# Kernel tuning notes

Measured on AMD Instinct MI355X. Metric: run time of the kernel, lower is better.

The kernel has to match this reference:

```python
import jax, jax.numpy as jnp
import numpy as np

B, H, W = 1, 180, 360
NB, BS = 8, 96
EMBED = NB * BS            # 768
LATENT = 4 * EMBED         # 3072 (mlp_ratio=4)
MODD = 64
LAM = 0.01                 # sparsity_threshold (softshrink)

def _ln(x, w, b):
    m = x.mean(-1, keepdims=True)
    v = x.var(-1, keepdims=True)
    return (x - m) * jax.lax.rsqrt(v + 1e-5) * w + b

def _gelu(x):
    return jax.nn.gelu(x, approximate=False)  # torch nn.GELU default (erf)

def _scale_shift(e, w0, b0, w1, b1):
    o = _gelu(e @ w0 + b0) @ w1 + b1
    s, t = jnp.split(o, 2, axis=1)
    return 1.0 + s, t

def _softshrink(x):
    return jnp.where(x > LAM, x - LAM, jnp.where(x < -LAM, x + LAM, 0.0))

def _bd(x, w):  # block-diagonal contraction on spectral features
    return jnp.einsum('nyxbi,bio->nyxbo', x, w)

def _filter(x, e, w1, b1, w2, b2, fs_w0, fs_b0, fs_w1, fs_b1):
    bias = x
    b, h, w, c = x.shape
    xf = jnp.fft.rfft2(x, axes=(1, 2), norm='ortho')
    wf = w // 2 + 1
    xr = xf.real.reshape(b, h, wf, NB, BS)
    xi = xf.imag.reshape(b, h, wf, NB, BS)
    tm = min(h, w) // 2 + 1
    km = tm  # hard_thresholding_fraction = 1.0
    lo, hi = tm - km, min(tm + km, h)
    xrk, xik = xr[:, lo:hi, :km], xi[:, lo:hi, :km]
    o1r = _bd(xrk, w1[0]) - _bd(xik, w1[1]) + b1[0]
    o1i = _bd(xik, w1[0]) + _bd(xrk, w1[1]) + b1[1]
    s, t = _scale_shift(e, fs_w0, fs_b0, fs_w1, fs_b1)  # 'real' mode
    s = s.reshape(b, 1, 1, NB, BS)
    t = t.reshape(b, 1, 1, NB, BS)
    o1r = jax.nn.relu(o1r * s + t)
    o1i = jax.nn.relu(o1i * s + t)
    o2r = _softshrink(_bd(o1r, w2[0]) - _bd(o1i, w2[1]) + b2[0])
    o2i = _softshrink(_bd(o1i, w2[0]) + _bd(o1r, w2[1]) + b2[1])
    full = jnp.zeros((b, h, wf, NB, BS), jnp.complex64)
    full = full.at[:, lo:hi, :km].set(o2r + 1j * o2i)
    out = jnp.fft.irfft2(full.reshape(b, h, wf, c), s=(h, w), axes=(1, 2), norm='ortho')
    return out + bias

def _mlp(x, e, fc1w, fc1b, fc2w, fc2b, ms_w0, ms_b0, ms_w1, ms_b1):
    s, t = _scale_shift(e, ms_w0, ms_b0, ms_w1, ms_b1)
    s = s[:, None, None, :]
    t = t[:, None, None, :]
    hmid = _gelu((x @ fc1w + fc1b) * s + t)
    return hmid @ fc2w + fc2b

def setup_inputs():
    key = jax.random.key(0)
    ks = jax.random.split(key, 16)
    g = lambda k, shp: 0.02 * jax.random.normal(k, shp, jnp.float32)
    return {
        'x': jax.random.normal(ks[0], (B, H, W, EMBED), jnp.float32),
        'mod_embed': jax.random.normal(ks[1], (B, MODD), jnp.float32),
        'n1w': jnp.ones((EMBED,), jnp.float32),
        'n1b': jnp.zeros((EMBED,), jnp.float32),
        'n2w': jnp.ones((EMBED,), jnp.float32),
        'n2b': jnp.zeros((EMBED,), jnp.float32),
        'w1': g(ks[2], (2, NB, BS, BS)),
        'b1': g(ks[3], (2, NB, BS)),
        'w2': g(ks[4], (2, NB, BS, BS)),
        'b2': g(ks[5], (2, NB, BS)),
        'fs_w0': g(ks[6], (MODD, 2 * EMBED)),
        'fs_b0': jnp.zeros((2 * EMBED,), jnp.float32),
        'fs_w1': g(ks[7], (2 * EMBED, 2 * EMBED)),
        'fs_b1': jnp.zeros((2 * EMBED,), jnp.float32),
        'fc1w': g(ks[8], (EMBED, LATENT)),
        'fc1b': jnp.zeros((LATENT,), jnp.float32),
        'fc2w': g(ks[9], (LATENT, EMBED)),
        'fc2b': jnp.zeros((EMBED,), jnp.float32),
        'ms_w0': g(ks[10], (MODD, 2 * LATENT)),
        'ms_b0': jnp.zeros((2 * LATENT,), jnp.float32),
        'ms_w1': g(ks[11], (2 * LATENT, 2 * LATENT)),
        'ms_b1': jnp.zeros((2 * LATENT,), jnp.float32),
    }

def reference(x, mod_embed, n1w, n1b, n2w, n2b, w1, b1, w2, b2,
              fs_w0, fs_b0, fs_w1, fs_b1, fc1w, fc1b, fc2w, fc2b,
              ms_w0, ms_b0, ms_w1, ms_b1):
    residual = x
    h = _ln(x, n1w, n1b)
    h = _filter(h, mod_embed, w1, b1, w2, b2, fs_w0, fs_b0, fs_w1, fs_b1)
    h = h + residual            # double_skip = True
    residual = h
    h2 = _ln(h, n2w, n2b)
    h2 = _mlp(h2, mod_embed, fc1w, fc1b, fc2w, fc2b, ms_w0, ms_b0, ms_w1, ms_b1)
    return h2 + residual
```

## Files before the change

kernel.cpp:

```cpp
#include <hip/hip_runtime.h>
#include <hip/hip_bf16.h>
#include <math.h>

#define HH 180
#define WW 360
#define CC 768
#define FF 91
#define NPOS (HH*FF)
#define NROW (HH*WW)
#define LAT 3072

typedef __attribute__((ext_vector_type(8))) short bf16x8;
typedef __attribute__((ext_vector_type(4))) float f32x4;
typedef __attribute__((ext_vector_type(4))) unsigned int u32x4;

__device__ __forceinline__ float gelu_f(float x) {
    return 0.5f * x * (1.0f + erff(x * 0.7071067811865476f));
}

__global__ __launch_bounds__(256) void mod_a_kernel(
        const float* __restrict__ e,
        const float* __restrict__ fs_w0, const float* __restrict__ fs_b0,
        const float* __restrict__ ms_w0, const float* __restrict__ ms_b0,
        float* __restrict__ mid_f, float* __restrict__ mid_m) {
    __shared__ float es[64];
    int t = threadIdx.x;
    if (t < 64) es[t] = e[t];
    __syncthreads();
    int j = blockIdx.x * 256 + t;
    if (j < 1536) {
        float a = fs_b0[j];
        #pragma unroll 8
        for (int k = 0; k < 64; k++) a += es[k] * fs_w0[k*1536 + j];
        mid_f[j] = gelu_f(a);
    } else {
        int jm = j - 1536;
        float a = ms_b0[jm];
        #pragma unroll 8
        for (int k = 0; k < 64; k++) a += es[k] * ms_w0[k*6144 + jm];
        mid_m[jm] = gelu_f(a);
    }
}

__global__ __launch_bounds__(512) void mod_b_kernel(
        const float* __restrict__ mid_f, const float* __restrict__ mid_m,
        const float* __restrict__ fs_w1, const float* __restrict__ fs_b1,
        const float* __restrict__ ms_w1, const float* __restrict__ ms_b1,
        float* __restrict__ s_f, float* __restrict__ t_f,
        float* __restrict__ s_m, float* __restrict__ t_m) {
    __shared__ float red[8*64];
    int t = threadIdx.x;
    int g = t >> 6;
    int jl = t & 63;
    int blk = blockIdx.x;
    if (blk < 24) {
        int jo = blk*64 + jl;
        const int N = 1536, NQ = 192;
        float a = 0.f;
        const float* w = fs_w1 + (size_t)(g*NQ)*N + jo;
        for (int j = 0; j < NQ; j++) a += mid_f[g*NQ + j] * w[(size_t)j*N];
        red[t] = a;
        __syncthreads();
        if (t < 64) {
            float s = fs_b1[jo];
            #pragma unroll
            for (int q = 0; q < 8; q++) s += red[q*64 + jl];
            if (jo < 768) s_f[jo] = 1.0f + s;
            else          t_f[jo - 768] = s;
        }
    } else {
        int jo = (blk - 24)*64 + jl;
        const int N = 6144, NQ = 768;
        float a = 0.f;
        const float* w = ms_w1 + (size_t)(g*NQ)*N + jo;
        for (int j = 0; j < NQ; j++) a += mid_m[g*NQ + j] * w[(size_t)j*N];
        red[t] = a;
        __syncthreads();
        if (t < 64) {
            float s = ms_b1[jo];
            #pragma unroll
            for (int q = 0; q < 8; q++) s += red[q*64 + jl];
            if (jo < 3072) s_m[jo] = 1.0f + s;
            else           t_m[jo - 3072] = s;
        }
    }
}

__global__ __launch_bounds__(256) void ln_bf16_kernel(const float* __restrict__ in,
        const float* __restrict__ w, const float* __restrict__ b,
        __hip_bfloat16* __restrict__ out) {
    int row = blockIdx.x*4 + (threadIdx.x >> 6);
    int l = threadIdx.x & 63;
    const float* p = in + (size_t)row*CC;
    float v[12]; float s = 0.f, sq = 0.f;
    #pragma unroll
    for (int i = 0; i < 12; i++) { float tv = p[l + 64*i]; v[i] = tv; s += tv; sq += tv*tv; }
    #pragma unroll
    for (int m = 1; m < 64; m <<= 1) { s += __shfl_xor(s, m); sq += __shfl_xor(sq, m); }
    float mean = s * (1.0f/768.0f);
    float var  = sq * (1.0f/768.0f) - mean*mean;
    float rstd = rsqrtf(var + 1e-5f);
    __hip_bfloat16* o = out + (size_t)row*CC;
    #pragma unroll
    for (int i = 0; i < 12; i++) { int c = l + 64*i; o[c] = __float2bfloat16((v[i]-mean)*rstd*w[c] + b[c]); }
}

__global__ __launch_bounds__(256) void ln_bf16in_kernel(const __hip_bfloat16* __restrict__ in,
        const float* __restrict__ w, const float* __restrict__ b,
        __hip_bfloat16* __restrict__ out) {
    int row = blockIdx.x*4 + (threadIdx.x >> 6);
    int l = threadIdx.x & 63;
    const __hip_bfloat16* p = in + (size_t)row*CC;
    float v[12]; float s = 0.f, sq = 0.f;
    #pragma unroll
    for (int i = 0; i < 12; i++) { float tv = __bfloat162float(p[l + 64*i]); v[i] = tv; s += tv; sq += tv*tv; }
    #pragma unroll
    for (int m = 1; m < 64; m <<= 1) { s += __shfl_xor(s, m); sq += __shfl_xor(sq, m); }
    float mean = s * (1.0f/768.0f);
    float var  = sq * (1.0f/768.0f) - mean*mean;
    float rstd = rsqrtf(var + 1e-5f);
    __hip_bfloat16* o = out + (size_t)row*CC;
    #pragma unroll
    for (int i = 0; i < 12; i++) { int c = l + 64*i; o[c] = __float2bfloat16((v[i]-mean)*rstd*w[c] + b[c]); }
}

__global__ __launch_bounds__(256) void ew_kernel(__hip_bfloat16* __restrict__ Ew) {
    int idx = blockIdx.x*256 + threadIdx.x;
    if (idx >= 192*384) return;
    int r = idx / 384, w = idx - (idx/384)*384;
    int f = (r < 96) ? r : r - 96;
    const float rn = 0.05270462766947299f;
    float v = 0.f;
    if (f < FF && w < WW) {
        int p = (f * w) % 360;
        float ang = 6.283185307179586f/360.0f * (float)p;
        float s_, c_; sincosf(ang, &s_, &c_);
        v = (r < 96) ? c_*rn : -s_*rn;
    }
    Ew[idx] = __float2bfloat16(v);
}

__global__ __launch_bounds__(256) void eh_kernel(__hip_bfloat16* __restrict__ Eh) {
    int idx = blockIdx.x*256 + threadIdx.x;
    if (idx >= 4*192*384) return;
    int sp = idx / (192*384);
    int rem = idx - sp*(192*384);
    int t = rem / 384, k = rem - (rem/384)*384;
    int sig = sp >> 1, plane = sp & 1;
    float s = (sig == 0) ? -1.f : 1.f;
    int h = (k < 192) ? k : k - 192;
    const float rnh = 0.07453559924999299f;
    float v = 0.f;
    if (t < HH && h < HH) {
        int p = (t * h) % 180;
        float ang = 6.283185307179586f/180.0f * (float)p;
        float s_, c_; sincosf(ang, &s_, &c_);
        float C = c_*rnh, S = s_*rnh;
        if (plane == 0) v = (k < 192) ? C : -s*S;
        else            v = (k < 192) ? s*S : C;
    }
    Eh[idx] = __float2bfloat16(v);
}

__global__ __launch_bounds__(256) void bdw_kernel(const float* __restrict__ w,
        __hip_bfloat16* __restrict__ Bt) {
    int idx = blockIdx.x*256 + threadIdx.x;
    if (idx >= 8*192*192) return;
    int wb = idx / (192*192);
    int rem = idx - wb*(192*192);
    int n2 = rem / 192, k2 = rem - (rem/192)*192;
    int k = (k2 < 96) ? k2 : k2 - 96;
    int oc = (n2 < 96) ? n2 : n2 - 96;
    float w0 = w[((size_t)wb*96 + k)*96 + oc];
    float w1v = w[((size_t)(8 + wb)*96 + k)*96 + oc];
    float v;
    if (n2 < 96) v = (k2 < 96) ? w0 : -w1v;
    else         v = (k2 < 96) ? w1v : w0;
    Bt[idx] = __float2bfloat16(v);
}

template<int MODE>
__global__ __launch_bounds__(256) void transform_mfma(
        const __hip_bfloat16* __restrict__ Amat,
        const __hip_bfloat16* __restrict__ B0, const __hip_bfloat16* __restrict__ B1,
        __hip_bfloat16* __restrict__ O0, __hip_bfloat16* __restrict__ O1) {
    __shared__ __align__(16) unsigned short As[192*72];
    __shared__ __align__(16) unsigned short Bs[128*72];
    int nbase = blockIdx.x * 128;
    int bat = blockIdx.z;
    int tid = threadIdx.x;
    int l = tid & 63, wv = tid >> 6;
    int wm = wv & 1, wn = wv >> 1;
    int lm = l & 15, kq = l >> 4;
    const __hip_bfloat16* Ab = Amat + (MODE == 1 ? (size_t)blockIdx.y*192*384 : 0);
    const __hip_bfloat16* pa[6];
    unsigned short* dsa[6];
    #pragma unroll
    for (int it = 0; it < 6; it++) {
        int ch = it*256 + tid;
        int row = ch >> 3, co = (ch & 7) * 8;
        pa[it]  = Ab + (size_t)row*384 + co;
        dsa[it] = As + row*72 + co;
    }
    const __hip_bfloat16* pb[4];
    int  brow[4];
    unsigned short* dsb[4];
    #pragma unroll
    for (int it = 0; it < 4; it++) {
        int idx = it*256 + tid;
        int row = idx >> 4;
        int cq = (idx & 15) * 8;
        brow[it] = row;
        dsb[it] = Bs + (size_t)cq*72 + row;
        if (MODE == 0) {
            pb[it] = B0 + (size_t)bat*WW*CC + (size_t)row*CC + nbase + cq;
        } else {
            pb[it] = nullptr;
        }
    }
    f32x4 acc[6][4] = {};
    for (int kt = 0; kt < 6; kt++) {
        int kb = kt*64;
        __syncthreads();
        #pragma unroll
        for (int it = 0; it < 6; it++) {
            u32x4 v = *(const u32x4*)(pa[it] + kb);
            *(u32x4*)(dsa[it]) = v;
        }
        #pragma unroll
        for (int it = 0; it < 4; it++) {
            int row = brow[it];
            int k = kb + row;
            unsigned int u[4] = {0u, 0u, 0u, 0u};
            if (MODE == 0) {
                if (k < WW) {
                    u32x4 v = *(const u32x4*)(pb[it] + (size_t)kb*CC);
                    u[0] = v[0]; u[1] = v[1]; u[2] = v[2]; u[3] = v[3];
                }
            } else {
                int idx = it*256 + tid;
                int cq = (idx & 15) * 8;
                if (k < 192) {
                    if (k < HH) {
                        u32x4 v = *(const u32x4*)(B0 + (size_t)k*FF*CC + (size_t)bat*CC + nbase + cq);
                        u[0] = v[0]; u[1] = v[1]; u[2] = v[2]; u[3] = v[3];
                    }
                } else {
                    int h2 = k - 192;
                    if (h2 < HH) {
                        u32x4 v = *(const u32x4*)(B1 + (size_t)h2*FF*CC + (size_t)bat*CC + nbase + cq);
                        u[0] = v[0]; u[1] = v[1]; u[2] = v[2]; u[3] = v[3];
                    }
                }
            }
            unsigned short* db = dsb[it];
            #pragma unroll
            for (int j = 0; j < 4; j++) {
                db[(2*j    )*72] = (unsigned short)(u[j] & 0xffffu);
                db[(2*j + 1)*72] = (unsigned short)(u[j] >> 16);
            }
        }
        __syncthreads();
        #pragma unroll
        for (int kk = 0; kk < 2; kk++) {
            int kg = kk*32 + kq*8;
            bf16x8 af[6], bfv[4];
            #pragma unroll
            for (int i = 0; i < 6; i++)
                af[i] = *(const bf16x8*)(As + (wm*96 + i*16 + lm)*72 + kg);
            #pragma unroll
            for (int j = 0; j < 4; j++)
                bfv[j] = *(const bf16x8*)(Bs + (wn*64 + j*16 + lm)*72 + kg);
            #pragma unroll
            for (int i = 0; i < 6; i++)
                #pragma unroll
                for (int j = 0; j < 4; j++)
                    acc[i][j] = __builtin_amdgcn_mfma_f32_16x16x32_bf16(af[i], bfv[j], acc[i][j], 0, 0, 0);
        }
    }
    int r0 = kq * 4;
    #pragma unroll
    for (int j = 0; j < 4; j++) {
        int col = nbase + wn*64 + j*16 + lm;
        #pragma unroll
        for (int i = 0; i < 6; i++) {
            #pragma unroll
            for (int r = 0; r < 4; r++) {
                int row = wm*96 + i*16 + r0 + r;
                __hip_bfloat16 hv = __float2bfloat16(acc[i][j][r]);
                if (MODE == 0) {
                    if (row < 96) {
                        if (row < FF) O0[(size_t)bat*FF*CC + (size_t)row*CC + col] = hv;
                    } else {
                        int f2 = row - 96;
                        if (f2 < FF) O1[(size_t)bat*FF*CC + (size_t)f2*CC + col] = hv;
                    }
                } else {
                    if (row < HH) {
                        __hip_bfloat16* Op = blockIdx.y ? O1 : O0;
                        Op[(size_t)row*FF*CC + (size_t)bat*CC + col] = hv;
                    }
                }
            }
        }
    }
}

template<int LAYER>
__global__ __launch_bounds__(384) void bd_mfma_kernel(
        const __hip_bfloat16* __restrict__ Ir, const __hip_bfloat16* __restrict__ Ii,
        const __hip_bfloat16* __restrict__ Bt,
        const float* __restrict__ bias,
        const float* __restrict__ sf, const float* __restrict__ tf,
        __hip_bfloat16* __restrict__ Or_, __hip_bfloat16* __restrict__ Oi_) {
    __shared__ __align__(16) unsigned short As[128*72];
    __shared__ __align__(16) unsigned short Bs[192*72];
    int mbase = blockIdx.x * 128;
    int wb = blockIdx.y;
    int tid = threadIdx.x;
    int l = tid & 63, wv = tid >> 6;
    int wm = wv & 1, wn = wv >> 1;
    int lm = l & 15, kq = l >> 4;
    const __hip_bfloat16* Bw = Bt + (size_t)wb*192*192;
    f32x4 acc[4][4] = {};
    for (int kt = 0; kt < 3; kt++) {
        __syncthreads();
        for (int ch = tid; ch < 1024; ch += 384) {
            int row = ch >> 3, q = ch & 7;
            int k2 = kt*64 + q*8;
            int p = mbase + row; if (p >= NPOS) p = NPOS - 1;
            const __hip_bfloat16* src = (k2 < 96) ? (Ir + (size_t)p*CC + wb*96 + k2)
                                                  : (Ii + (size_t)p*CC + wb*96 + (k2 - 96));
            *(u32x4*)(As + row*72 + q*8) = *(const u32x4*)src;
        }
        for (int ch = tid; ch < 1536; ch += 384) {
            int row = ch >> 3, co = (ch & 7) * 8;
            u32x4 v = *(const u32x4*)(Bw + (size_t)row*192 + kt*64 + co);
            *(u32x4*)(Bs + row*72 + co) = v;
        }
        __syncthreads();
        #pragma unroll
        for (int kk = 0; kk < 2; kk++) {
            int kg = kk*32 + kq*8;
            bf16x8 af[4], bfv[4];
            #pragma unroll
            for (int i = 0; i < 4; i++) {
                af[i]  = *(const bf16x8*)(As + (wm*64 + i*16 + lm)*72 + kg);
                bfv[i] = *(const bf16x8*)(Bs + (wn*64 + i*16 + lm)*72 + kg);
            }
            #pragma unroll
            for (int i = 0; i < 4; i++)
                #pragma unroll
                for (int j = 0; j < 4; j++)
                    acc[i][j] = __builtin_amdgcn_mfma_f32_16x16x32_bf16(af[i], bfv[j], acc[i][j], 0, 0, 0);
        }
    }
    int r0 = kq * 4;
    #pragma unroll
    for (int j = 0; j < 4; j++) {
        int n2 = wn*64 + j*16 + lm;
        int oc = (n2 < 96) ? n2 : n2 - 96;
        float bb = bias[((n2 < 96) ? 0 : 768) + wb*96 + oc];
        float ss = 0.f, tt = 0.f;
        if (LAYER == 0) { ss = sf[wb*96 + oc]; tt = tf[wb*96 + oc]; }
        __hip_bfloat16* Op = (n2 < 96) ? Or_ : Oi_;
        #pragma unroll
        for (int i = 0; i < 4; i++) {
            #pragma unroll
            for (int r = 0; r < 4; r++) {
                int p = mbase + wm*64 + i*16 + r0 + r;
                if (p < NPOS) {
                    float v = acc[i][j][r] + bb;
                    if (LAYER == 0) {
                        v = fmaxf(v*ss + tt, 0.0f);
                    } else {
                        v = (v > 0.01f) ? (v - 0.01f) : ((v < -0.01f) ? (v + 0.01f) : 0.0f);
                    }
                    Op[(size_t)p*CC + wb*96 + oc] = __float2bfloat16(v);
                }
            }
        }
    }
}

__global__ __launch_bounds__(256) void aw_kernel(__hip_bfloat16* __restrict__ Aw) {
    int idx = blockIdx.x*256 + threadIdx.x;
    if (idx >= 384*96) return;
    int w = idx / 96, f = idx - (idx/96)*96;
    const float rn = 0.05270462766947299f;
    float m = (f == 0) ? rn : ((f < FF) ? 2.0f*rn : 0.0f);
    int p = (int)(((long long)f * w) % 360);
    float ang = 6.283185307179586f / 360.0f * (float)p;
    float s_, c_; sincosf(ang, &s_, &c_);
    Aw[idx]          = __float2bfloat16(m * c_);
    Aw[384*96 + idx] = __float2bfloat16(-m * s_);
}

__global__ __launch_bounds__(256) void iwdft_mfma_kernel(
        const __hip_bfloat16* __restrict__ Zr, const __hip_bfloat16* __restrict__ Zi,
        const __hip_bfloat16* __restrict__ Aw,
        const __hip_bfloat16* __restrict__ hlnb,
        const float* __restrict__ xin, __hip_bfloat16* __restrict__ hbf) {
    __shared__ __align__(16) unsigned short As[128*104];
    __shared__ __align__(16) unsigned short Bs[128*104];
    int h = blockIdx.z;
    int mbase = blockIdx.y * 128;
    int nbase = blockIdx.x * 128;
    int tid = threadIdx.x;
    int l = tid & 63, wv = tid >> 6;
    int wm = wv & 1, wn = wv >> 1;
    int lm = l & 15, kq = l >> 4;
    f32x4 acc[4][4] = {};
    #pragma unroll
    for (int ph = 0; ph < 2; ph++) {
        __syncthreads();
        for (int ch = tid; ch < 1536; ch += 256) {
            int row = ch / 12, co = (ch - row*12) * 8;
            u32x4 v = *(const u32x4*)(Aw + ((size_t)ph*384 + mbase + row)*96 + co);
            *(u32x4*)(As + row*104 + co) = v;
        }
        const __hip_bfloat16* Zp = ph ? Zi : Zr;
        for (int ch = tid; ch < 1536; ch += 256) {
            int f = ch >> 4, cq = (ch & 15) * 8;
            unsigned int u[4] = {0u, 0u, 0u, 0u};
            if (f < FF) {
                u32x4 v = *(const u32x4*)(Zp + ((size_t)h*FF + f)*CC + nbase + cq);
                u[0] = v[0]; u[1] = v[1]; u[2] = v[2]; u[3] = v[3];
            }
            #pragma unroll
            for (int j = 0; j < 4; j++) {
                Bs[(cq + 2*j    )*104 + f] = (unsigned short)(u[j] & 0xffffu);
                Bs[(cq + 2*j + 1)*104 + f] = (unsigned short)(u[j] >> 16);
            }
        }
        __syncthreads();
        #pragma unroll
        for (int ks = 0; ks < 3; ks++) {
            int kg = ks*32 + kq*8;
            bf16x8 af[4], bfv[4];
            #pragma unroll
            for (int i = 0; i < 4; i++) {
                af[i]  = *(const bf16x8*)(As + (wm*64 + i*16 + lm)*104 + kg);
                bfv[i] = *(const bf16x8*)(Bs + (wn*64 + i*16 + lm)*104 + kg);
            }
            #pragma unroll
            for (int i = 0; i < 4; i++)
                #pragma unroll
                for (int j = 0; j < 4; j++)
                    acc[i][j] = __builtin_amdgcn_mfma_f32_16x16x32_bf16(af[i], bfv[j], acc[i][j], 0, 0, 0);
        }
    }
    int r0 = kq * 4;
    #pragma unroll
    for (int j = 0; j < 4; j++) {
        int col = nbase + wn*64 + j*16 + lm;
        #pragma unroll
        for (int i = 0; i < 4; i++) {
            int rowb = wm*64 + i*16 + r0;
            #pragma unroll
            for (int r = 0; r < 4; r++) {
                int wp = mbase + rowb + r;
                if (wp < WW) {
                    size_t idx = ((size_t)h*WW + wp)*CC + col;
                    float v = acc[i][j][r] + __bfloat162float(hlnb[idx]) + xin[idx];
                    hbf[idx] = __float2bfloat16(v);
                }
            }
        }
    }
}

__global__ __launch_bounds__(256) void transpose_bf16_kernel(const float* __restrict__ src,
        __hip_bfloat16* __restrict__ dst, int K, int N) {
    __shared__ float tile[32][33];
    int n0 = blockIdx.x * 32;
    int k0 = blockIdx.y * 32;
    int tx = threadIdx.x & 31;
    int ty = threadIdx.x >> 5;
    #pragma unroll
    for (int r = 0; r < 32; r += 8) {
        tile[ty + r][tx] = src[(size_t)(k0 + ty + r) * N + n0 + tx];
    }
    __syncthreads();
    #pragma unroll
    for (int r = 0; r < 32; r += 8) {
        dst[(size_t)(n0 + ty + r) * K + k0 + tx] = __float2bfloat16(tile[tx][ty + r]);
    }
}

template<int MODE>
__global__ __launch_bounds__(512, 2) void gemm256_kernel(
        const __hip_bfloat16* __restrict__ A,
        const __hip_bfloat16* __restrict__ Bt,
        int M, int K, int N,
        const float* __restrict__ bias,
        const float* __restrict__ sv, const float* __restrict__ tv,
        const void* resid, void* out) {
    __shared__ __align__(16) unsigned short SH[65536];
    unsigned short* Asb = SH;
    unsigned short* Bsb = SH + 32768;
    int tid = threadIdx.x;
    int nwg = gridDim.x;
    int q8 = nwg >> 3, r8 = nwg & 7;
    int bid = blockIdx.x;
    int xcd = bid & 7;
    int lid = ((xcd < r8) ? xcd*(q8 + 1) : r8*(q8 + 1) + (xcd - r8)*q8) + (bid >> 3);
    int nx = N >> 8;
    int by = lid / nx;
    int bx = lid - by*nx;
    int nbase = bx << 8;
    int mbase = by << 8;
    int l = tid & 63, wv = tid >> 6;
    int wm = wv & 1, wn = wv >> 1;
    int lm = l & 15, kq = l >> 4;
    f32x4 acc[8][4] = {};
    int nkt = K >> 6;

    const __hip_bfloat16* pga[4];
    const __hip_bfloat16* pgb[4];
    int ldso[4];
    #pragma unroll
    for (int i = 0; i < 4; i++) {
        int ch = i*512 + tid;
        int row = ch >> 3;
        int sl = ch & 7;
        int kg = (sl ^ (row & 7)) << 3;
        int am = mbase + row; if (am >= M) am = M - 1;
        pga[i] = A  + (size_t)am * K + kg;
        pgb[i] = Bt + (size_t)(nbase + row) * K + kg;
        ldso[i] = ch*8;
    }
    auto stage = [&](int d, int kt) {
        int kb = kt << 6;
        int db = d*16384;
        #pragma unroll
        for (int i = 0; i < 4; i++) {
            __builtin_amdgcn_global_load_lds(
                (const __attribute__((address_space(1))) void*)(unsigned long long)(uintptr_t)(pga[i] + kb),
                (__attribute__((address_space(3))) void*)(unsigned long long)(uintptr_t)(Asb + db + ldso[i]),
                16, 0, 0);
            __builtin_amdgcn_global_load_lds(
                (const __attribute__((address_space(1))) void*)(unsigned long long)(uintptr_t)(pgb[i] + kb),
                (__attribute__((address_space(3))) void*)(unsigned long long)(uintptr_t)(Bsb + db + ldso[i]),
                16, 0, 0);
        }
    };

    stage(0, 0);
    __syncthreads();
    for (int kt = 0; kt < nkt; kt++) {
        if (kt + 1 < nkt) stage((kt + 1) & 1, kt + 1);
        int d = kt & 1;
        const unsigned short* Ab = Asb + d*16384;
        const unsigned short* Bb = Bsb + d*16384;
        #pragma unroll
        for (int kk = 0; kk < 2; kk++) {
            bf16x8 af[8], bfv[4];
            #pragma unroll
            for (int i = 0; i < 8; i++) {
                int ra = wm*128 + i*16 + lm;
                af[i] = *(const bf16x8*)(Ab + ra*64 + ((((kk<<2)+kq) ^ (ra&7))<<3));
            }
            #pragma unroll
            for (int j = 0; j < 4; j++) {
                int rb = wn*64 + j*16 + lm;
                bfv[j] = *(const bf16x8*)(Bb + rb*64 + ((((kk<<2)+kq) ^ (rb&7))<<3));
            }
            #pragma unroll
            for (int i = 0; i < 8; i++)
                #pragma unroll
                for (int j = 0; j < 4; j++)
                    acc[i][j] = __builtin_amdgcn_mfma_f32_16x16x32_bf16(af[i], bfv[j], acc[i][j], 0, 0, 0);
        }
        __syncthreads();
    }

    int r0 = kq * 4;
    if (MODE == 0) {
        #pragma unroll
        for (int j = 0; j < 4; j++) {
            int col = wn*64 + j*16 + lm;
            int gcol = nbase + col;
            float bb = bias[gcol];
            float ss = sv[gcol], tt = tv[gcol];
            #pragma unroll
            for (int i = 0; i < 8; i++) {
                int rowb = wm*128 + i*16 + r0;
                #pragma unroll
                for (int r = 0; r < 4; r++) {
                    float v = gelu_f((acc[i][j][r] + bb)*ss + tt);
                    __hip_bfloat16 hb = __float2bfloat16(v);
                    SH[(rowb + r)*256 + col] = *reinterpret_cast<unsigned short*>(&hb);
                }
            }
        }
        __syncthreads();
        #pragma unroll
        for (int it = 0; it < 16; it++) {
            int chunk = it*512 + tid;
            int row = chunk >> 5;
            int c8 = chunk & 31;
            int mr = mbase + row;
            if (mr < M) {
                *(u32x4*)((__hip_bfloat16*)out + (size_t)mr*N + nbase + c8*8) =
                    *(const u32x4*)(SH + row*256 + c8*8);
            }
        }
    } else {
        const __hip_bfloat16* rb16 = (const __hip_bfloat16*)resid;
        #pragma unroll
        for (int j = 0; j < 4; j++) {
            int col = nbase + wn*64 + j*16 + lm;
            float bb = bias[col];
            #pragma unroll
            for (int i = 0; i < 8; i++) {
                int rowb = mbase + wm*128 + i*16 + r0;
                #pragma unroll
                for (int r = 0; r < 4; r++) {
                    int row = rowb + r;
                    if (row < M) {
                        float v = acc[i][j][r] + bb;
                        ((float*)out)[(size_t)row*N + col] =
                            v + __bfloat162float(rb16[(size_t)row*N + col]);
                    }
                }
            }
        }
    }
}

extern "C" void kernel_launch(void* const* d_in, const int* in_sizes, int n_in,
                              void* d_out, int out_size, void* d_ws, size_t ws_size,
                              hipStream_t stream) {
    const float* x     = (const float*)d_in[0];
    const float* emb   = (const float*)d_in[1];
    const float* n1w   = (const float*)d_in[2];
    const float* n1b   = (const float*)d_in[3];
    const float* n2w   = (const float*)d_in[4];
    const float* n2b   = (const float*)d_in[5];
    const float* w1    = (const float*)d_in[6];
    const float* b1    = (const float*)d_in[7];
    const float* w2    = (const float*)d_in[8];
    const float* b2    = (const float*)d_in[9];
    const float* fs_w0 = (const float*)d_in[10];
    const float* fs_b0 = (const float*)d_in[11];
    const float* fs_w1 = (const float*)d_in[12];
    const float* fs_b1 = (const float*)d_in[13];
    const float* fc1w  = (const float*)d_in[14];
    const float* fc1b  = (const float*)d_in[15];
    const float* fc2w  = (const float*)d_in[16];
    const float* fc2b  = (const float*)d_in[17];
    const float* ms_w0 = (const float*)d_in[18];
    const float* ms_b0 = (const float*)d_in[19];
    const float* ms_w1 = (const float*)d_in[20];
    const float* ms_b1 = (const float*)d_in[21];
    float* out = (float*)d_out;
    (void)in_sizes; (void)n_in; (void)out_size; (void)ws_size;

    char* wsb = (char*)d_ws;
    size_t off = 0;
    auto alloc = [&](size_t nbytes) -> void* {
        void* p = wsb + off;
        off += (nbytes + 255) & ~(size_t)255;
        return p;
    };
    float* s_f  = (float*)alloc(768*4);
    float* t_f  = (float*)alloc(768*4);
    float* s_m  = (float*)alloc(3072*4);
    float* t_m  = (float*)alloc(3072*4);
    float* midf = (float*)alloc(1536*4);
    float* midm = (float*)alloc(6144*4);
    __hip_bfloat16* Aw  = (__hip_bfloat16*)alloc((size_t)2*384*96*2);
    __hip_bfloat16* Ew  = (__hip_bfloat16*)alloc((size_t)192*384*2);
    __hip_bfloat16* Eh  = (__hip_bfloat16*)alloc((size_t)4*192*384*2);
    __hip_bfloat16* Bt1 = (__hip_bfloat16*)alloc((size_t)8*192*192*2);
    __hip_bfloat16* Bt2 = (__hip_bfloat16*)alloc((size_t)8*192*192*2);
    __hip_bfloat16* Yrb = (__hip_bfloat16*)alloc((size_t)NPOS*CC*2);
    __hip_bfloat16* Yib = (__hip_bfloat16*)alloc((size_t)NPOS*CC*2);
    __hip_bfloat16* Zrb = (__hip_bfloat16*)alloc((size_t)NPOS*CC*2);
    __hip_bfloat16* Zib = (__hip_bfloat16*)alloc((size_t)NPOS*CC*2);
    __hip_bfloat16* wT1  = (__hip_bfloat16*)alloc((size_t)CC*LAT*2);
    __hip_bfloat16* wT2  = (__hip_bfloat16*)alloc((size_t)CC*LAT*2);
    __hip_bfloat16* h2   = (__hip_bfloat16*)alloc((size_t)NROW*CC*2);
    __hip_bfloat16* hbf  = (__hip_bfloat16*)alloc((size_t)NROW*CC*2);
    __hip_bfloat16* hmid = (__hip_bfloat16*)alloc((size_t)NROW*LAT*2);
    __hip_bfloat16* hlnb = h2;

    mod_a_kernel<<<30, 256, 0, stream>>>(emb, fs_w0, fs_b0, ms_w0, ms_b0, midf, midm);
    mod_b_kernel<<<120, 512, 0, stream>>>(midf, midm, fs_w1, fs_b1, ms_w1, ms_b1,
                                          s_f, t_f, s_m, t_m);
    aw_kernel<<<144, 256, 0, stream>>>(Aw);
    ew_kernel<<<288, 256, 0, stream>>>(Ew);
    eh_kernel<<<1152, 256, 0, stream>>>(Eh);
    bdw_kernel<<<1152, 256, 0, stream>>>(w1, Bt1);
    bdw_kernel<<<1152, 256, 0, stream>>>(w2, Bt2);
    ln_bf16_kernel<<<NROW/4, 256, 0, stream>>>(x, n1w, n1b, hlnb);
    transpose_bf16_kernel<<<dim3(LAT/32, CC/32), 256, 0, stream>>>(fc1w, wT1, 768, 3072);
    transpose_bf16_kernel<<<dim3(CC/32, LAT/32), 256, 0, stream>>>(fc2w, wT2, 3072, 768);

    transform_mfma<0><<<dim3(6, 1, 180), 256, 0, stream>>>(Ew, hlnb, nullptr, Yrb, Yib);
    transform_mfma<1><<<dim3(6, 2, 91), 256, 0, stream>>>(Eh, Yrb, Yib, Zrb, Zib);
    bd_mfma_kernel<0><<<dim3(128, 8), 384, 0, stream>>>(Zrb, Zib, Bt1, b1, s_f, t_f, Yrb, Yib);
    bd_mfma_kernel<1><<<dim3(128, 8), 384, 0, stream>>>(Yrb, Yib, Bt2, b2, nullptr, nullptr, Zrb, Zib);
    transform_mfma<1><<<dim3(6, 2, 91), 256, 0, stream>>>(Eh + (size_t)2*192*384, Zrb, Zib, Yrb, Yib);
    iwdft_mfma_kernel<<<dim3(6, 3, 180), 256, 0, stream>>>(Yrb, Yib, Aw, hlnb, x, hbf);

    ln_bf16in_kernel<<<NROW/4, 256, 0, stream>>>(hbf, n2w, n2b, h2);
    gemm256_kernel<0><<<dim3((LAT/256) * ((NROW+255)/256)), 512, 0, stream>>>(
        h2, wT1, NROW, CC, LAT, fc1b, s_m, t_m, nullptr, hmid);
    gemm256_kernel<1><<<dim3((CC/256) * ((NROW+255)/256)), 512, 0, stream>>>(
        hmid, wT2, NROW, LAT, CC, fc2b, nullptr, nullptr, hbf, out);
}
```

Before: 1.838 ms.

## Use triple-buffered BK=32 LDS pipeline with explicit vmcnt waits in GEMM

The 256x256 GEMM now uses a K-tile of 32 with three LDS buffers (96KB instead of 128KB) and prefetches two tiles ahead. Fine-grained s_waitcnt vmcnt plus raw barriers replace the __syncthreads-per-tile scheme. The MODE 0 epilogue writes the output tile in two 128-row halves with padded row stride 264 to fit the smaller LDS and cut bank conflicts. The aim is deeper overlap of global-to-LDS loads with MFMA, and lower LDS use that may help occupancy. The cost is twice as many barriers per K and hand-written waitcnt counts that must match the number of outstanding loads.

```diff
diff --git a/kernel.cpp b/kernel.cpp
--- a/kernel.cpp
+++ b/kernel.cpp
@@ -496,9 +496,7 @@
         const float* __restrict__ bias,
         const float* __restrict__ sv, const float* __restrict__ tv,
         const void* resid, void* out) {
-    __shared__ __align__(16) unsigned short SH[65536];
-    unsigned short* Asb = SH;
-    unsigned short* Bsb = SH + 32768;
+    __shared__ __align__(16) unsigned short SH[49152];
     int tid = threadIdx.x;
     int nwg = gridDim.x;
     int q8 = nwg >> 3, r8 = nwg & 7;
@@ -514,97 +512,112 @@
     int wm = wv & 1, wn = wv >> 1;
     int lm = l & 15, kq = l >> 4;
     f32x4 acc[8][4] = {};
-    int nkt = K >> 6;
-
-    const __hip_bfloat16* pga[4];
-    const __hip_bfloat16* pgb[4];
-    int ldso[4];
-    #pragma unroll
-    for (int i = 0; i < 4; i++) {
+    int nkt = K >> 5;
+
+    const __hip_bfloat16* pga[2];
+    const __hip_bfloat16* pgb[2];
+    int ldso[2];
+    #pragma unroll
+    for (int i = 0; i < 2; i++) {
         int ch = i*512 + tid;
-        int row = ch >> 3;
-        int sl = ch & 7;
-        int kg = (sl ^ (row & 7)) << 3;
+        int row = ch >> 2;
+        int sl = ch & 3;
+        int kg = (sl ^ (row & 3)) << 3;
         int am = mbase + row; if (am >= M) am = M - 1;
         pga[i] = A  + (size_t)am * K + kg;
         pgb[i] = Bt + (size_t)(nbase + row) * K + kg;
         ldso[i] = ch*8;
     }
-    auto stage = [&](int d, int kt) {
-        int kb = kt << 6;
-        int db = d*16384;
-        #pragma unroll
-        for (int i = 0; i < 4; i++) {
+    auto stage = [&](int b, int kt) {
+        int kb = kt << 5;
+        int db = b*16384;
+        #pragma unroll
+        for (int i = 0; i < 2; i++) {
             __builtin_amdgcn_global_load_lds(
                 (const __attribute__((address_space(1))) void*)(unsigned long long)(uintptr_t)(pga[i] + kb),
-                (__attribute__((address_space(3))) void*)(unsigned long long)(uintptr_t)(Asb + db + ldso[i]),
+                (__attribute__((address_space(3))) void*)(unsigned long long)(uintptr_t)(SH + db + ldso[i]),
                 16, 0, 0);
             __builtin_amdgcn_global_load_lds(
                 (const __attribute__((address_space(1))) void*)(unsigned long long)(uintptr_t)(pgb[i] + kb),
-                (__attribute__((address_space(3))) void*)(unsigned long long)(uintptr_t)(Bsb + db + ldso[i]),
+                (__attribute__((address_space(3))) void*)(unsigned long long)(uintptr_t)(SH + db + 8192 + ldso[i]),
                 16, 0, 0);
         }
     };
 
     stage(0, 0);
-    __syncthreads();
+    stage(1, 1);
+    int bcur = 0;
     for (int kt = 0; kt < nkt; kt++) {
-        if (kt + 1 < nkt) stage((kt + 1) & 1, kt + 1);
-        int d = kt & 1;
-        const unsigned short* Ab = Asb + d*16384;
-        const unsigned short* Bb = Bsb + d*16384;
-        #pragma unroll
-        for (int kk = 0; kk < 2; kk++) {
-            bf16x8 af[8], bfv[4];
-            #pragma unroll
-            for (int i = 0; i < 8; i++) {
-                int ra = wm*128 + i*16 + lm;
-                af[i] = *(const bf16x8*)(Ab + ra*64 + ((((kk<<2)+kq) ^ (ra&7))<<3));
-            }
-            #pragma unroll
-            for (int j = 0; j < 4; j++) {
-                int rb = wn*64 + j*16 + lm;
-                bfv[j] = *(const bf16x8*)(Bb + rb*64 + ((((kk<<2)+kq) ^ (rb&7))<<3));
-            }
-            #pragma unroll
-            for (int i = 0; i < 8; i++)
-                #pragma unroll
-                for (int j = 0; j < 4; j++)
-                    acc[i][j] = __builtin_amdgcn_mfma_f32_16x16x32_bf16(af[i], bfv[j], acc[i][j], 0, 0, 0);
-        }
-        __syncthreads();
+        if (kt + 2 < nkt) {
+            int bnxt = bcur + 2; if (bnxt >= 3) bnxt -= 3;
+            stage(bnxt, kt + 2);
+            asm volatile("s_waitcnt vmcnt(8)" ::: "memory");
+        } else if (kt + 1 < nkt) {
+            asm volatile("s_waitcnt vmcnt(4)" ::: "memory");
+        } else {
+            asm volatile("s_waitcnt vmcnt(0)" ::: "memory");
+        }
+        __builtin_amdgcn_s_barrier();
+        asm volatile("" ::: "memory");
+        const unsigned short* Ab = SH + bcur*16384;
+        const unsigned short* Bb = SH + bcur*16384 + 8192;
+        bf16x8 af[8], bfv[4];
+        #pragma unroll
+        for (int i = 0; i < 8; i++) {
+            int ra = wm*128 + i*16 + lm;
+            af[i] = *(const bf16x8*)(Ab + ra*32 + ((kq ^ (ra&3))<<3));
+        }
+        #pragma unroll
+        for (int j = 0; j < 4; j++) {
+            int rb = wn*64 + j*16 + lm;
+            bfv[j] = *(const bf16x8*)(Bb + rb*32 + ((kq ^ (rb&3))<<3));
+        }
+        #pragma unroll
+        for (int i = 0; i < 8; i++)
+            #pragma unroll
+            for (int j = 0; j < 4; j++)
+                acc[i][j] = __builtin_amdgcn_mfma_f32_16x16x32_bf16(af[i], bfv[j], acc[i][j], 0, 0, 0);
+        asm volatile("" ::: "memory");
+        __builtin_amdgcn_s_barrier();
+        bcur = (bcur == 2) ? 0 : bcur + 1;
     }
 
     int r0 = kq * 4;
     if (MODE == 0) {
         #pragma unroll
-        for (int j = 0; j < 4; j++) {
-            int col = wn*64 + j*16 + lm;
-            int gcol = nbase + col;
-            float bb = bias[gcol];
-            float ss = sv[gcol], tt = tv[gcol];
-            #pragma unroll
-            for (int i = 0; i < 8; i++) {
-                int rowb = wm*128 + i*16 + r0;
+        for (int p = 0; p < 2; p++) {
+            if (wm == p) {
                 #pragma unroll
-                for (int r = 0; r < 4; r++) {
-                    float v = gelu_f((acc[i][j][r] + bb)*ss + tt);
-                    __hip_bfloat16 hb = __float2bfloat16(v);
-                    SH[(rowb + r)*256 + col] = *reinterpret_cast<unsigned short*>(&hb);
+                for (int j = 0; j < 4; j++) {
+                    int col = wn*64 + j*16 + lm;
+                    int gcol = nbase + col;
+                    float bb = bias[gcol];
+                    float ss = sv[gcol], tt = tv[gcol];
+                    #pragma unroll
+                    for (int i = 0; i < 8; i++) {
+                        int rl = i*16 + r0;
+                        #pragma unroll
+                        for (int r = 0; r < 4; r++) {
+                            float v = gelu_f((acc[i][j][r] + bb)*ss + tt);
+                            __hip_bfloat16 hb = __float2bfloat16(v);
+                            SH[(rl + r)*264 + col] = *reinterpret_cast<unsigned short*>(&hb);
+                        }
+                    }
                 }
             }
-        }
-        __syncthreads();
-        #pragma unroll
-        for (int it = 0; it < 16; it++) {
-            int chunk = it*512 + tid;
-            int row = chunk >> 5;
-            int c8 = chunk & 31;
-            int mr = mbase + row;
-            if (mr < M) {
-                *(u32x4*)((__hip_bfloat16*)out + (size_t)mr*N + nbase + c8*8) =
-                    *(const u32x4*)(SH + row*256 + c8*8);
-            }
+            __syncthreads();
+            #pragma unroll
+            for (int it = 0; it < 8; it++) {
+                int chunk = it*512 + tid;
+                int row = chunk >> 5;
+                int c8 = chunk & 31;
+                int mr = mbase + p*128 + row;
+                if (mr < M) {
+                    *(u32x4*)((__hip_bfloat16*)out + (size_t)mr*N + nbase + c8*8) =
+                        *(const u32x4*)(SH + row*264 + c8*8);
+                }
+            }
+            __syncthreads();
         }
     } else {
         const __hip_bfloat16* rb16 = (const __hip_bfloat16*)resid;
```

Result: slower. 2.090 ms (+13.7%).
